# Kernel tuning notes

Measured on AMD Instinct MI355X. Metric: run time of the kernel, lower is better.

The kernel has to match this reference:

```python
import jax, jax.numpy as jnp
import numpy as np

T, D, H, AE, DFF, B = 128, 256, 8, 32, 512, 256
EPS = 1e-5


def _xavier(key, shape):
    fan_in, fan_out = shape[-2], shape[-1]
    limit = float(np.sqrt(6.0 / (fan_in + fan_out)))
    return jax.random.uniform(key, shape, jnp.float32, -limit, limit)


def setup_inputs() -> dict:
    key = jax.random.key(0)
    ks = jax.random.split(key, 9)
    return {
        "X": jax.random.normal(ks[0], (B, T, D), jnp.float32),
        "Q": _xavier(ks[1], (T, D, H * AE)),
        "K": _xavier(ks[2], (T, D, H * AE)),
        "V": _xavier(ks[3], (T, D, H * D)),
        "O": _xavier(ks[4], (T, H * D, D)),
        "W_gate": _xavier(ks[5], (T, D, DFF)),
        "W_up": _xavier(ks[6], (T, D, DFF)),
        "W_down": _xavier(ks[7], (T, DFF, D)),
        "gamma1": jnp.ones((D,), jnp.float32),
        "beta1": jnp.zeros((D,), jnp.float32),
        "gamma2": jnp.ones((D,), jnp.float32),
        "beta2": jnp.zeros((D,), jnp.float32),
    }


def _layer_norm(x, gamma, beta):
    mu = jnp.mean(x, axis=-1, keepdims=True)
    var = jnp.mean((x - mu) ** 2, axis=-1, keepdims=True)
    return (x - mu) * jax.lax.rsqrt(var + EPS) * gamma + beta


def reference(X, Q, K, V, O, W_gate, W_up, W_down, gamma1, beta1, gamma2, beta2):
    b, t, d = X.shape
    # --- heterogeneous self-attention (dropout is identity in eval mode) ---
    q = jnp.einsum('btd,tde->bte', X, Q).reshape(b, t, H, AE)
    k = jnp.einsum('btd,tde->bte', X, K).reshape(b, t, H, AE)
    v = jnp.einsum('btd,tdn->btn', X, V).reshape(b, t, H, d)
    scores = jnp.einsum('bthe,bshe->bhts', q, k) / jnp.sqrt(jnp.float32(AE))
    attn = jax.nn.softmax(scores, axis=-1)
    out = jnp.einsum('bhts,bshd->bthd', attn, v).reshape(b, t, H * d)
    attn_out = jnp.einsum('btn,tnd->btd', out, O)
    x = _layer_norm(X + attn_out, gamma1, beta1)
    # --- token-specific SwishGLU FFN ---
    gate = jnp.einsum('btd,tdf->btf', x, W_gate)
    up = jnp.einsum('btd,tdf->btf', x, W_up)
    hidden = jax.nn.silu(gate) * up
    ffn_out = jnp.einsum('btf,tfd->btd', hidden, W_down)
    return _layer_norm(x + ffn_out, gamma2, beta2)
```

## Files before the change

kernel.cpp:

```cpp
#include <hip/hip_runtime.h>
#include <stdint.h>

#define DEVI static __device__ __forceinline__

typedef __attribute__((ext_vector_type(4))) float f32x4;
typedef __attribute__((ext_vector_type(8))) short bf8;
typedef __attribute__((ext_vector_type(4))) unsigned short u16x4;

DEVI unsigned short f2bf(float f) {
  unsigned u = __builtin_bit_cast(unsigned, f);
  u = (u + 0x7FFFu + ((u >> 16) & 1u)) >> 16;
  return (unsigned short)u;
}
DEVI float bf2f(unsigned short s) {
  return __builtin_bit_cast(float, ((unsigned)s) << 16);
}
DEVI unsigned cvt_pk_bf16(float lo, float hi) {
  unsigned r;
  asm("v_cvt_pk_bf16_f32 %0, %1, %2" : "=v"(r) : "v"(lo), "v"(hi));
  return r;
}
DEVI int swz(int row) { return (((row >> 2) ^ row) & 7) << 4; }
DEVI int swz32(int row) { return (((row >> 1) ^ row) & 3) << 4; }

DEVI void gload16(const void* g, void* l) {
  __builtin_amdgcn_global_load_lds(
      (const __attribute__((address_space(1))) unsigned*)g,
      (__attribute__((address_space(3))) unsigned*)l, 16, 0, 0);
}

template<bool OUT_BF16>
__global__ __launch_bounds__(512, 4)
void gemm_tk(const unsigned short* __restrict__ A, const float* __restrict__ W0,
             const float* __restrict__ W1, void* __restrict__ C,
             int Ka, int N, int lognx, int ldC)
{
  const int j = blockIdx.x;
  const int t = (j & 7) + ((j >> (3 + lognx)) << 3);
  const int nblk = (j >> 3) & ((1 << lognx) - 1);
  const int n0blk = nblk * 128;
  const float* Wsel = (n0blk >= N) ? W1 : W0;
  const int n0w = (n0blk >= N) ? (n0blk - N) : n0blk;

  const int tid = threadIdx.x;
  const int lane = tid & 63;
  const int wv = tid >> 6;
  const int wrow = wv * 32;

  __shared__ short As[2][256 * 32];
  __shared__ short Ws[2][128 * 32];

  f32x4 acc[2][8];
#pragma unroll
  for (int i = 0; i < 2; ++i)
#pragma unroll
    for (int jj = 0; jj < 8; ++jj) acc[i][jj] = f32x4{0.f, 0.f, 0.f, 0.f};

  const long ldA = 128L * Ka;
  const unsigned short* Ab = A + (long)t * Ka;
  const float* Wb = Wsel + (long)t * Ka * N + n0w;

  const int n0 = (tid & 31) * 4;
  const int kp = tid >> 5;

#pragma unroll
  for (int it = 0; it < 2; ++it) {
    int ci = tid + it * 512;
    int m = ci >> 2, cb = (ci & 3) * 16;
    gload16((const char*)(Ab + (long)m * ldA) + (cb ^ swz32(m)),
            (char*)(&As[0][0]) + ci * 16);
  }
  {
    f32x4 wlo = *(const f32x4*)(Wb + (long)(kp * 2) * N + n0);
    f32x4 whi = *(const f32x4*)(Wb + (long)(kp * 2 + 1) * N + n0);
#pragma unroll
    for (int jj = 0; jj < 4; ++jj) {
      int n = n0 + jj;
      *(unsigned*)((char*)(&Ws[0][0]) + n * 64 + ((kp * 4) ^ swz32(n))) =
          cvt_pk_bf16(wlo[jj], whi[jj]);
    }
  }

  const int nt = Ka >> 5;
  int cur = 0;
  for (int kt = 0; kt < nt; ++kt) {
    __syncthreads();
    const bool more = (kt + 1) < nt;
    f32x4 wlo, whi;
    if (more) {
      const unsigned short* An = Ab + (kt + 1) * 32;
#pragma unroll
      for (int it = 0; it < 2; ++it) {
        int ci = tid + it * 512;
        int m = ci >> 2, cb = (ci & 3) * 16;
        gload16((const char*)(An + (long)m * ldA) + (cb ^ swz32(m)),
                (char*)(&As[cur ^ 1][0]) + ci * 16);
      }
      const float* Wn = Wb + (long)(kt + 1) * 32 * N;
      wlo = *(const f32x4*)(Wn + (long)(kp * 2) * N + n0);
      whi = *(const f32x4*)(Wn + (long)(kp * 2 + 1) * N + n0);
    }
    const int kb2 = (lane >> 4) * 16;
    bf8 a0, a1;
    {
      const int m0 = wrow + (lane & 15);
      const int m1 = m0 + 16;
      a0 = *(const bf8*)((const char*)(&As[cur][0]) + m0 * 64 + (kb2 ^ swz32(m0)));
      a1 = *(const bf8*)((const char*)(&As[cur][0]) + m1 * 64 + (kb2 ^ swz32(m1)));
    }
#pragma unroll
    for (int ni = 0; ni < 8; ++ni) {
      const int n = ni * 16 + (lane & 15);
      bf8 bfr = *(const bf8*)((const char*)(&Ws[cur][0]) + n * 64 + (kb2 ^ swz32(n)));
      acc[0][ni] = __builtin_amdgcn_mfma_f32_16x16x32_bf16(a0, bfr, acc[0][ni], 0, 0, 0);
      acc[1][ni] = __builtin_amdgcn_mfma_f32_16x16x32_bf16(a1, bfr, acc[1][ni], 0, 0, 0);
    }
    if (more) {
#pragma unroll
      for (int jj = 0; jj < 4; ++jj) {
        int n = n0 + jj;
        *(unsigned*)((char*)(&Ws[cur ^ 1][0]) + n * 64 + ((kp * 4) ^ swz32(n))) =
            cvt_pk_bf16(wlo[jj], whi[jj]);
      }
    }
    cur ^= 1;
  }
#pragma unroll
  for (int mi = 0; mi < 2; ++mi)
#pragma unroll
    for (int ni = 0; ni < 8; ++ni)
#pragma unroll
      for (int r = 0; r < 4; ++r) {
        int m = wrow + mi * 16 + (lane >> 4) * 4 + r;
        int n = n0blk + ni * 16 + (lane & 15);
        long off = ((long)m * 128 + t) * ldC + n;
        float v = acc[mi][ni][r];
        if constexpr (OUT_BF16) reinterpret_cast<unsigned short*>(C)[off] = f2bf(v);
        else reinterpret_cast<float*>(C)[off] = v;
      }
}

__global__ __launch_bounds__(256)
void cvt_bf(const float* __restrict__ in, unsigned short* __restrict__ out, long n)
{
  long i = ((long)blockIdx.x * 256 + threadIdx.x) * 8;
  if (i >= n) return;
  f32x4 a = *reinterpret_cast<const f32x4*>(in + i);
  f32x4 b = *reinterpret_cast<const f32x4*>(in + i + 4);
  u16x4 w0, w1;
#pragma unroll
  for (int j = 0; j < 4; ++j) { w0[j] = f2bf(a[j]); w1[j] = f2bf(b[j]); }
  *reinterpret_cast<u16x4*>(out + i) = w0;
  *reinterpret_cast<u16x4*>(out + i + 4) = w1;
}

__global__ __launch_bounds__(256)
void trans_v(const unsigned short* __restrict__ vb, unsigned short* __restrict__ vT)
{
  const int bh = blockIdx.y;
  const int b = bh >> 3, h = bh & 7;
  const int tile = blockIdx.x;
  const int tt = tile >> 3;
  const int td = tile & 7;
  __shared__ unsigned short sm[32][33];
  const int rloc = threadIdx.x >> 3;
  const int q4 = (threadIdx.x & 7) * 4;
  {
    long off = ((long)b * 128 + tt * 32 + rloc) * 2048 + h * 256 + td * 32 + q4;
    u16x4 v = *reinterpret_cast<const u16x4*>(vb + off);
#pragma unroll
    for (int j = 0; j < 4; ++j) sm[rloc][q4 + j] = v[j];
  }
  __syncthreads();
  {
    u16x4 w;
#pragma unroll
    for (int j = 0; j < 4; ++j) w[j] = sm[q4 + j][rloc];
    long off = ((long)bh * 256 + td * 32 + rloc) * 128 + tt * 32 + q4;
    *reinterpret_cast<u16x4*>(vT + off) = w;
  }
}

__global__ __launch_bounds__(512, 4)
void attn_k(const unsigned short* __restrict__ qk, const unsigned short* __restrict__ vT,
            unsigned short* __restrict__ cat)
{
  const int h = blockIdx.x, b = blockIdx.y;
  const int tid = threadIdx.x, lane = tid & 63, wv = tid >> 6;
  const int wrow = wv * 16;

  __shared__ short ps[128 * 128];
  __shared__ short vs[2][256 * 32];

  const long qkBase = ((long)b * 128) * 512 + h * 32;
  const long vBase = ((long)(b * 8 + h)) * 256 * 128;
  const int kb_ = (lane >> 4) * 8;

#pragma unroll
  for (int it = 0; it < 2; ++it) {
    int ci = tid + it * 512;
    int d = ci >> 2, sc = ci & 3;
    gload16(vT + vBase + (long)d * 128 + (((sc * 16) ^ swz32(d)) >> 1),
            (char*)(&vs[0][0]) + ci * 16);
  }

  f32x4 sacc[8];
#pragma unroll
  for (int c = 0; c < 8; ++c) sacc[c] = f32x4{0.f, 0.f, 0.f, 0.f};
  bf8 aq;
  {
    int row = wrow + (lane & 15);
    aq = *reinterpret_cast<const bf8*>(qk + qkBase + (long)row * 512 + kb_);
  }
#pragma unroll
  for (int ni = 0; ni < 8; ++ni) {
    int s = ni * 16 + (lane & 15);
    bf8 bk = *reinterpret_cast<const bf8*>(qk + qkBase + 256 + (long)s * 512 + kb_);
    sacc[ni] = __builtin_amdgcn_mfma_f32_16x16x32_bf16(aq, bk, sacc[ni], 0, 0, 0);
  }

  const float scale = 0.17677669529663687f;
  float sinv[4];
#pragma unroll
  for (int r = 0; r < 4; ++r) {
    int row = wrow + (lane >> 4) * 4 + r;
    float vv[8];
    float mx = -1e30f;
#pragma unroll
    for (int c = 0; c < 8; ++c) { vv[c] = sacc[c][r] * scale; mx = fmaxf(mx, vv[c]); }
#pragma unroll
    for (int mm = 1; mm < 16; mm <<= 1) mx = fmaxf(mx, __shfl_xor(mx, mm, 64));
    float s_ = 0.f;
#pragma unroll
    for (int c = 0; c < 8; ++c) { vv[c] = __expf(vv[c] - mx); s_ += vv[c]; }
#pragma unroll
    for (int mm = 1; mm < 16; mm <<= 1) s_ += __shfl_xor(s_, mm, 64);
    sinv[r] = 1.0f / s_;
#pragma unroll
    for (int c = 0; c < 8; ++c) {
      int col = c * 16 + (lane & 15);
      int byte = row * 256 + ((col * 2) ^ swz(row));
      *reinterpret_cast<unsigned short*>(reinterpret_cast<char*>(ps) + byte) = f2bf(vv[c]);
    }
  }

  f32x4 oacc[16];
#pragma unroll
  for (int c = 0; c < 16; ++c) oacc[c] = f32x4{0.f, 0.f, 0.f, 0.f};

#pragma unroll 1
  for (int cs = 0; cs < 4; ++cs) {
    __syncthreads();
    if (cs < 3) {
#pragma unroll
      for (int it = 0; it < 2; ++it) {
        int ci = tid + it * 512;
        int d = ci >> 2, sc = ci & 3;
        gload16(vT + vBase + (long)d * 128 + (cs + 1) * 32 + (((sc * 16) ^ swz32(d)) >> 1),
                (char*)(&vs[(cs + 1) & 1][0]) + ci * 16);
      }
    }
    const int kglob = cs * 32 + kb_;
    bf8 ap;
    {
      int row = wrow + (lane & 15);
      int byte = row * 256 + ((kglob * 2) ^ swz(row));
      ap = *reinterpret_cast<const bf8*>(reinterpret_cast<const char*>(ps) + byte);
    }
    __builtin_amdgcn_s_setprio(1);
#pragma unroll
    for (int c = 0; c < 16; ++c) {
      int d = c * 16 + (lane & 15);
      bf8 bv = *reinterpret_cast<const bf8*>(
          reinterpret_cast<const char*>(&vs[cs & 1][0]) + d * 64 + ((kb_ * 2) ^ swz32(d)));
      oacc[c] = __builtin_amdgcn_mfma_f32_16x16x32_bf16(ap, bv, oacc[c], 0, 0, 0);
    }
    __builtin_amdgcn_s_setprio(0);
  }

#pragma unroll
  for (int c = 0; c < 16; ++c)
#pragma unroll
    for (int r = 0; r < 4; ++r) {
      int tt = wrow + (lane >> 4) * 4 + r;
      int d = c * 16 + (lane & 15);
      float v = oacc[c][r] * sinv[r];
      long off = ((long)b * 128 + tt) * 2048 + h * 256 + d;
      cat[off] = f2bf(v);
    }
}

template<bool WF, bool WB>
__global__ __launch_bounds__(256)
void ln_k(const unsigned short* __restrict__ a, const unsigned short* __restrict__ bsrc,
          const float* __restrict__ gamma, const float* __restrict__ beta,
          float* __restrict__ of, unsigned short* __restrict__ ob)
{
  const int row = blockIdx.x * 4 + (threadIdx.x >> 6);
  const int lane = threadIdx.x & 63;
  const long base = (long)row * 256 + lane * 4;
  u16x4 ua = *reinterpret_cast<const u16x4*>(a + base);
  u16x4 ub = *reinterpret_cast<const u16x4*>(bsrc + base);
  f32x4 x;
#pragma unroll
  for (int j = 0; j < 4; ++j) x[j] = bf2f(ua[j]) + bf2f(ub[j]);
  float s = x[0] + x[1] + x[2] + x[3];
  float s2 = x[0] * x[0] + x[1] * x[1] + x[2] * x[2] + x[3] * x[3];
#pragma unroll
  for (int mm = 1; mm < 64; mm <<= 1) { s += __shfl_xor(s, mm, 64); s2 += __shfl_xor(s2, mm, 64); }
  float mean = s * (1.f / 256.f);
  float var = fmaxf(s2 * (1.f / 256.f) - mean * mean, 0.f);
  float inv = rsqrtf(var + 1e-5f);
  f32x4 g = *reinterpret_cast<const f32x4*>(gamma + lane * 4);
  f32x4 be = *reinterpret_cast<const f32x4*>(beta + lane * 4);
  f32x4 y;
#pragma unroll
  for (int j = 0; j < 4; ++j) y[j] = (x[j] - mean) * inv * g[j] + be[j];
  if constexpr (WF) *reinterpret_cast<f32x4*>(of + base) = y;
  if constexpr (WB) {
    u16x4 w;
#pragma unroll
    for (int j = 0; j < 4; ++j) w[j] = f2bf(y[j]);
    *reinterpret_cast<u16x4*>(ob + base) = w;
  }
}

__global__ __launch_bounds__(256)
void silu_k(const unsigned short* __restrict__ gu, unsigned short* __restrict__ o, long n)
{
  long i = ((long)blockIdx.x * 256 + threadIdx.x) * 8;
  if (i >= n) return;
  long r = i >> 9;
  int f = (int)(i & 511);
  const unsigned short* g = gu + r * 1024 + f;
  const unsigned short* u = g + 512;
  u16x4 g0 = *reinterpret_cast<const u16x4*>(g);
  u16x4 g1 = *reinterpret_cast<const u16x4*>(g + 4);
  u16x4 u0 = *reinterpret_cast<const u16x4*>(u);
  u16x4 u1 = *reinterpret_cast<const u16x4*>(u + 4);
  u16x4 o0, o1;
#pragma unroll
  for (int j = 0; j < 4; ++j) {
    float gg = bf2f(g0[j]), uu = bf2f(u0[j]);
    o0[j] = f2bf(gg / (1.f + __expf(-gg)) * uu);
    gg = bf2f(g1[j]); uu = bf2f(u1[j]);
    o1[j] = f2bf(gg / (1.f + __expf(-gg)) * uu);
  }
  *reinterpret_cast<u16x4*>(o + i) = o0;
  *reinterpret_cast<u16x4*>(o + i + 4) = o1;
}

extern "C" void kernel_launch(void* const* d_in, const int* in_sizes, int n_in,
                              void* d_out, int out_size, void* d_ws, size_t ws_size,
                              hipStream_t stream)
{
  const float* X  = (const float*)d_in[0];
  const float* Qw = (const float*)d_in[1];
  const float* Kw = (const float*)d_in[2];
  const float* Vw = (const float*)d_in[3];
  const float* Ow = (const float*)d_in[4];
  const float* Wg = (const float*)d_in[5];
  const float* Wu = (const float*)d_in[6];
  const float* Wd = (const float*)d_in[7];
  const float* g1 = (const float*)d_in[8];
  const float* b1 = (const float*)d_in[9];
  const float* g2 = (const float*)d_in[10];
  const float* b2 = (const float*)d_in[11];

  char* ws = (char*)d_ws;
  const size_t MiB = 1048576;
  unsigned short* Xb  = (unsigned short*)(ws);
  unsigned short* qkb = (unsigned short*)(ws + 16 * MiB);
  char* regA = ws + 48 * MiB;
  char* regB = regA + 128 * MiB;

  unsigned short* vb     = (unsigned short*)regA;
  unsigned short* vT     = (unsigned short*)regB;
  unsigned short* cat    = (unsigned short*)regA;
  unsigned short* attnpb = (unsigned short*)(regB);
  unsigned short* x1b    = (unsigned short*)(regB + 16 * MiB);
  unsigned short* ffnb   = (unsigned short*)(regB + 32 * MiB);
  unsigned short* gateup = (unsigned short*)(regA);
  unsigned short* hidb   = (unsigned short*)(regA + 64 * MiB);
  float* out = (float*)d_out;

  dim3 blk(256), gblk(512);
  cvt_bf<<<dim3(4096), blk, 0, stream>>>(X, Xb, (long)8388608);
  gemm_tk<true><<<dim3(512), gblk, 0, stream>>>(Xb, Qw, Kw, (void*)qkb, 256, 256, 2, 512);
  gemm_tk<true><<<dim3(2048), gblk, 0, stream>>>(Xb, Vw, Vw, (void*)vb, 256, 2048, 4, 2048);
  trans_v<<<dim3(32, 2048), blk, 0, stream>>>(vb, vT);
  attn_k<<<dim3(8, 256), gblk, 0, stream>>>(qkb, vT, cat);
  gemm_tk<true><<<dim3(256), gblk, 0, stream>>>(cat, Ow, Ow, (void*)attnpb, 2048, 256, 1, 256);
  ln_k<false, true><<<dim3(8192), blk, 0, stream>>>(Xb, attnpb, g1, b1, (float*)nullptr, x1b);
  gemm_tk<true><<<dim3(1024), gblk, 0, stream>>>(x1b, Wg, Wu, (void*)gateup, 256, 512, 3, 1024);
  silu_k<<<dim3(8192), blk, 0, stream>>>(gateup, hidb, (long)16777216);
  gemm_tk<true><<<dim3(256), gblk, 0, stream>>>(hidb, Wd, Wd, (void*)ffnb, 512, 256, 1, 256);
  ln_k<true, false><<<dim3(8192), blk, 0, stream>>>(x1b, ffnb, g2, b2, out, (unsigned short*)nullptr);
}
```

Measured before the change: 541.4 us.

## Keep attention probabilities in registers via transposed QK MFMA and lane shuffles

The QK^T MFMA operands are swapped so each lane holds a column of scores, which lets the softmax reduce with two cross-lane shuffles. The probabilities are normalized before being packed to bf16, then rearranged into the PV A-operand layout with ds_bpermute shuffles rather than a round trip through a 32KB LDS buffer. This removes LDS traffic and frees shared memory, which could raise occupancy. In exchange it adds shuffle and select instructions in each PV step, and rounding the normalized probabilities to bf16 slightly changes numerics.

```diff
diff --git a/kernel.cpp b/kernel.cpp
--- a/kernel.cpp
+++ b/kernel.cpp
@@ -6,6 +6,7 @@
 typedef __attribute__((ext_vector_type(4))) float f32x4;
 typedef __attribute__((ext_vector_type(8))) short bf8;
 typedef __attribute__((ext_vector_type(4))) unsigned short u16x4;
+typedef __attribute__((ext_vector_type(4))) unsigned int u32x4;
 
 DEVI unsigned short f2bf(float f) {
   unsigned u = __builtin_bit_cast(unsigned, f);
@@ -20,7 +21,6 @@
   asm("v_cvt_pk_bf16_f32 %0, %1, %2" : "=v"(r) : "v"(lo), "v"(hi));
   return r;
 }
-DEVI int swz(int row) { return (((row >> 2) ^ row) & 7) << 4; }
 DEVI int swz32(int row) { return (((row >> 1) ^ row) & 3) << 4; }
 
 DEVI void gload16(const void* g, void* l) {
@@ -189,7 +189,6 @@
   const int tid = threadIdx.x, lane = tid & 63, wv = tid >> 6;
   const int wrow = wv * 16;
 
-  __shared__ short ps[128 * 128];
   __shared__ short vs[2][256 * 32];
 
   const long qkBase = ((long)b * 128) * 512 + h * 32;
@@ -216,37 +215,42 @@
   for (int ni = 0; ni < 8; ++ni) {
     int s = ni * 16 + (lane & 15);
     bf8 bk = *reinterpret_cast<const bf8*>(qk + qkBase + 256 + (long)s * 512 + kb_);
-    sacc[ni] = __builtin_amdgcn_mfma_f32_16x16x32_bf16(aq, bk, sacc[ni], 0, 0, 0);
+    sacc[ni] = __builtin_amdgcn_mfma_f32_16x16x32_bf16(bk, aq, sacc[ni], 0, 0, 0);
   }
 
   const float scale = 0.17677669529663687f;
-  float sinv[4];
-#pragma unroll
-  for (int r = 0; r < 4; ++r) {
-    int row = wrow + (lane >> 4) * 4 + r;
-    float vv[8];
-    float mx = -1e30f;
-#pragma unroll
-    for (int c = 0; c < 8; ++c) { vv[c] = sacc[c][r] * scale; mx = fmaxf(mx, vv[c]); }
-#pragma unroll
-    for (int mm = 1; mm < 16; mm <<= 1) mx = fmaxf(mx, __shfl_xor(mx, mm, 64));
-    float s_ = 0.f;
-#pragma unroll
-    for (int c = 0; c < 8; ++c) { vv[c] = __expf(vv[c] - mx); s_ += vv[c]; }
-#pragma unroll
-    for (int mm = 1; mm < 16; mm <<= 1) s_ += __shfl_xor(s_, mm, 64);
-    sinv[r] = 1.0f / s_;
-#pragma unroll
-    for (int c = 0; c < 8; ++c) {
-      int col = c * 16 + (lane & 15);
-      int byte = row * 256 + ((col * 2) ^ swz(row));
-      *reinterpret_cast<unsigned short*>(reinterpret_cast<char*>(ps) + byte) = f2bf(vv[c]);
-    }
+  float mx = -1e30f;
+#pragma unroll
+  for (int ni = 0; ni < 8; ++ni)
+#pragma unroll
+    for (int r = 0; r < 4; ++r) { sacc[ni][r] *= scale; mx = fmaxf(mx, sacc[ni][r]); }
+  mx = fmaxf(mx, __shfl_xor(mx, 16, 64));
+  mx = fmaxf(mx, __shfl_xor(mx, 32, 64));
+  float s_ = 0.f;
+#pragma unroll
+  for (int ni = 0; ni < 8; ++ni)
+#pragma unroll
+    for (int r = 0; r < 4; ++r) { float e = __expf(sacc[ni][r] - mx); sacc[ni][r] = e; s_ += e; }
+  s_ += __shfl_xor(s_, 16, 64);
+  s_ += __shfl_xor(s_, 32, 64);
+  const float sinv = 1.0f / s_;
+
+  unsigned pk[8][2];
+#pragma unroll
+  for (int ni = 0; ni < 8; ++ni) {
+    pk[ni][0] = cvt_pk_bf16(sacc[ni][0] * sinv, sacc[ni][1] * sinv);
+    pk[ni][1] = cvt_pk_bf16(sacc[ni][2] * sinv, sacc[ni][3] * sinv);
   }
 
   f32x4 oacc[16];
 #pragma unroll
   for (int c = 0; c < 16; ++c) oacc[c] = f32x4{0.f, 0.f, 0.f, 0.f};
+
+  const int p = lane >> 4;
+  const int colL = lane & 15;
+  const int src0 = (2 * (p & 1) + 0) * 16 + colL;
+  const int src1 = (2 * (p & 1) + 1) * 16 + colL;
+  const bool hiSel = (lane & 32) != 0;
 
 #pragma unroll 1
   for (int cs = 0; cs < 4; ++cs) {
@@ -260,12 +264,23 @@
                 (char*)(&vs[(cs + 1) & 1][0]) + ci * 16);
       }
     }
-    const int kglob = cs * 32 + kb_;
     bf8 ap;
     {
-      int row = wrow + (lane & 15);
-      int byte = row * 256 + ((kglob * 2) ^ swz(row));
-      ap = *reinterpret_cast<const bf8*>(reinterpret_cast<const char*>(ps) + byte);
+      const int kst = cs;
+      unsigned lo0 = __shfl(pk[2 * kst][0], src0, 64);
+      unsigned lo1 = __shfl(pk[2 * kst][1], src0, 64);
+      unsigned lo2 = __shfl(pk[2 * kst][0], src1, 64);
+      unsigned lo3 = __shfl(pk[2 * kst][1], src1, 64);
+      unsigned hi0 = __shfl(pk[2 * kst + 1][0], src0, 64);
+      unsigned hi1 = __shfl(pk[2 * kst + 1][1], src0, 64);
+      unsigned hi2 = __shfl(pk[2 * kst + 1][0], src1, 64);
+      unsigned hi3 = __shfl(pk[2 * kst + 1][1], src1, 64);
+      u32x4 W;
+      W[0] = hiSel ? hi0 : lo0;
+      W[1] = hiSel ? hi1 : lo1;
+      W[2] = hiSel ? hi2 : lo2;
+      W[3] = hiSel ? hi3 : lo3;
+      ap = __builtin_bit_cast(bf8, W);
     }
     __builtin_amdgcn_s_setprio(1);
 #pragma unroll
@@ -284,7 +299,7 @@
     for (int r = 0; r < 4; ++r) {
       int tt = wrow + (lane >> 4) * 4 + r;
       int d = c * 16 + (lane & 15);
-      float v = oacc[c][r] * sinv[r];
+      float v = oacc[c][r];
       long off = ((long)b * 128 + tt) * 2048 + h * 256 + d;
       cat[off] = f2bf(v);
     }
```

Result: slower. 563.6 us (+4.1%).
